# Kernel optimization log

Measured on AMD Instinct MI355X. Metric: run time of the kernel, lower is better.

Reference implementation:

```python
import jax, jax.numpy as jnp
import numpy as np

NUM_EMBEDDINGS = 1024
EMBEDDING_DIM = 256
COMMITMENT_COST = 0.25


def setup_inputs() -> dict:
    key = jax.random.key(0)
    k1, k2 = jax.random.split(key)
    inputs = jax.random.normal(k1, (64, 256, 32, 32), dtype=jnp.float32)
    # nn.Embedding weight init: uniform(-1/K, 1/K)
    embedding = jax.random.uniform(
        k2, (NUM_EMBEDDINGS, EMBEDDING_DIM), dtype=jnp.float32,
        minval=-1.0 / NUM_EMBEDDINGS, maxval=1.0 / NUM_EMBEDDINGS)
    return {"inputs": inputs, "embedding": embedding}


def reference(inputs, embedding):
    # NCHW -> NHWC, flatten to [N, D]
    x = jnp.transpose(inputs, (0, 2, 3, 1))  # [B,H,W,D]
    input_shape = x.shape
    flat = x.reshape(-1, EMBEDDING_DIM)  # [N, D]

    # squared euclidean distances to all codebook entries: [N, K]
    distances = (jnp.sum(flat ** 2, axis=1, keepdims=True)
                 + jnp.sum(embedding ** 2, axis=1)
                 - 2.0 * flat @ embedding.T)
    idx = jnp.argmin(distances, axis=1)  # [N]

    # one-hot encodings (returned output); quantization via gather is
    # mathematically identical to encodings @ embedding
    encodings = jax.nn.one_hot(idx, NUM_EMBEDDINGS, dtype=embedding.dtype)  # [N,K]
    quantized_flat = embedding[idx]  # [N, D]
    quantized = quantized_flat.reshape(input_shape)  # [B,H,W,D]

    e_latent_loss = jnp.mean((jax.lax.stop_gradient(quantized) - x) ** 2)
    q_latent_loss = jnp.mean((quantized - jax.lax.stop_gradient(x)) ** 2)
    loss = q_latent_loss + COMMITMENT_COST * e_latent_loss

    # straight-through estimator
    quantized_st = x + jax.lax.stop_gradient(quantized - x)

    avg_probs = jnp.mean(encodings, axis=0)  # [K]
    perplexity = jnp.exp(-jnp.sum(avg_probs * jnp.log(avg_probs + 1e-10)))

    quantized_out = jnp.transpose(quantized_st, (0, 3, 1, 2))  # NHWC -> NCHW
    return (loss, quantized_out, perplexity, encodings, quantized_flat)
```

## Files before the change

kernel.cpp:

```cpp
#include <hip/hip_runtime.h>
#include <hip/hip_bf16.h>
#include <math.h>

#define NB    64
#define D     256
#define K     1024
#define HW    1024
#define NTOT  65536
#define MARGIN 1e-4f

#define OUT_QOUT   1
#define OUT_PERP   16777217
#define OUT_ENC    16777218
#define OUT_QFLAT  83886082


typedef __attribute__((ext_vector_type(8))) short bf16x8;
typedef __attribute__((ext_vector_type(4))) float f32x4;

__global__ void enorm_kernel(const float* __restrict__ emb, float* __restrict__ enorm) {
    int k = blockIdx.x * 256 + threadIdx.x;
    const float4* row = (const float4*)(emb + (size_t)k * D);
    float s = 0.f;
    #pragma unroll
    for (int q = 0; q < D / 4; q++) {
        float4 v = row[q];
        s += v.x * v.x + v.y * v.y + v.z * v.z + v.w * v.w;
    }
    enorm[k] = s;
}

__global__ void esplit_kernel(const float* __restrict__ emb, ushort* __restrict__ efrag) {
    const int ntg = blockIdx.x;
    const int t = threadIdx.x;
    __shared__ float sEm[16 * 260];

    {
        const int row = t >> 4, seg = t & 15;
        const float4* src = (const float4*)(emb + (size_t)(ntg * 16 + row) * D + seg * 16);
        float4* dst = (float4*)(sEm + row * 260 + seg * 16);
        #pragma unroll
        for (int q = 0; q < 4; q++) dst[q] = src[q];
    }
    __syncthreads();

    const int w = t >> 6, lane = t & 63;
    for (int fb = w; fb < 16; fb += 4) {
        const int h = fb >> 3, dc = fb & 7;
        const float* srcp = sEm + (lane & 15) * 260 + dc * 32 + (lane >> 4) * 8;
        ushort o[8];
        #pragma unroll
        for (int j = 0; j < 8; j++) {
            float x = srcp[j];
            __hip_bfloat16 hb = __float2bfloat16(x);
            if (h == 0) { o[j] = *(ushort*)&hb; }
            else {
                float hf = __bfloat162float(hb);
                __hip_bfloat16 lb = __float2bfloat16(x - hf);
                o[j] = *(ushort*)&lb;
            }
        }
        ushort* dst = efrag + ((size_t)(h * 64 + ntg) * 8 + dc) * 512 + lane * 8;
        *(int4*)dst = *(int4*)o;
    }
}

__global__ __launch_bounds__(256, 2) void score_mfma_kernel(
    const float* __restrict__ in, const ushort* __restrict__ efrag,
    const float* __restrict__ enorm, int* __restrict__ idx,
    int* __restrict__ rcount, int* __restrict__ rlist)
{
    __shared__ ushort sA[32768];

    const int t = threadIdx.x;
    const int n0 = blockIdx.x * 64;
    const int b = n0 >> 10, p0 = n0 & 1023;

    {
        const float* src = in + (size_t)b * (D * HW) + (size_t)t * HW + p0;
        const int quad = (t >> 3) & 3, dc = t >> 5, j = t & 7;
        #pragma unroll
        for (int g = 0; g < 4; g++) {
            float xs[16];
            #pragma unroll
            for (int q = 0; q < 4; q++) {
                float4 v = ((const float4*)src)[g * 4 + q];
                xs[q * 4 + 0] = v.x; xs[q * 4 + 1] = v.y; xs[q * 4 + 2] = v.z; xs[q * 4 + 3] = v.w;
            }
            #pragma unroll
            for (int mm = 0; mm < 16; mm++) {
                float x = xs[mm];
                __hip_bfloat16 hb = __float2bfloat16(x);
                float hf = __bfloat162float(hb);
                __hip_bfloat16 lb = __float2bfloat16(x - hf);
                const int l = mm + 16 * quad;
                sA[((0 * 4 + g) * 8 + dc) * 512 + l * 8 + j] = *(ushort*)&hb;
                sA[((1 * 4 + g) * 8 + dc) * 512 + l * 8 + j] = *(ushort*)&lb;
            }
        }
    }
    __syncthreads();

    const int w = t >> 6, lane = t & 63;

    float rm1 = 3.4e38f, rm2 = 3.4e38f; int ri = 0;

    for (int kp = 0; kp < 4; kp++) {
        float env[4]; int kc[4];
        #pragma unroll
        for (int ntl = 0; ntl < 4; ntl++) {
            kc[ntl] = kp * 256 + (w * 4 + ntl) * 16 + (lane & 15);
            env[ntl] = enorm[kc[ntl]];
        }
        f32x4 acc[4][4];
        #pragma unroll
        for (int mt = 0; mt < 4; mt++)
            #pragma unroll
            for (int ntl = 0; ntl < 4; ntl++) acc[mt][ntl] = (f32x4){0.f, 0.f, 0.f, 0.f};

        bf16x8 bh[4], bl[4], nbh[4], nbl[4];
        {
            #pragma unroll
            for (int ntl = 0; ntl < 4; ntl++) {
                const int ntg = kp * 16 + w * 4 + ntl;
                const size_t off = ((size_t)ntg * 8 + 0) * 512 + lane * 8;
                bh[ntl] = *(const bf16x8*)(efrag + off);
                bl[ntl] = *(const bf16x8*)(efrag + off + 262144);
            }
        }
        for (int dc = 0; dc < 8; dc++) {
            if (dc < 7) {
                #pragma unroll
                for (int ntl = 0; ntl < 4; ntl++) {
                    const int ntg = kp * 16 + w * 4 + ntl;
                    const size_t off = ((size_t)ntg * 8 + dc + 1) * 512 + lane * 8;
                    nbh[ntl] = *(const bf16x8*)(efrag + off);
                    nbl[ntl] = *(const bf16x8*)(efrag + off + 262144);
                }
            }
            #pragma unroll
            for (int mt = 0; mt < 4; mt++) {
                bf16x8 ah = *(const bf16x8*)(sA + ((0 * 4 + mt) * 8 + dc) * 512 + lane * 8);
                bf16x8 al = *(const bf16x8*)(sA + ((1 * 4 + mt) * 8 + dc) * 512 + lane * 8);
                #pragma unroll
                for (int ntl = 0; ntl < 4; ntl++) {
                    acc[mt][ntl] = __builtin_amdgcn_mfma_f32_16x16x32_bf16(al, bh[ntl], acc[mt][ntl], 0, 0, 0);
                    acc[mt][ntl] = __builtin_amdgcn_mfma_f32_16x16x32_bf16(ah, bl[ntl], acc[mt][ntl], 0, 0, 0);
                    acc[mt][ntl] = __builtin_amdgcn_mfma_f32_16x16x32_bf16(ah, bh[ntl], acc[mt][ntl], 0, 0, 0);
                }
            }
            if (dc < 7) {
                #pragma unroll
                for (int ntl = 0; ntl < 4; ntl++) { bh[ntl] = nbh[ntl]; bl[ntl] = nbl[ntl]; }
            }
        }

        #pragma unroll
        for (int mt = 0; mt < 4; mt++)
            #pragma unroll
            for (int r = 0; r < 4; r++) {
                float m1 = 3.4e38f, m2 = 3.4e38f; int i1 = 0;
                #pragma unroll
                for (int ntl = 0; ntl < 4; ntl++) {
                    float s = env[ntl] - 2.0f * acc[mt][ntl][r];
                    if (s < m1) { m2 = m1; m1 = s; i1 = kc[ntl]; }
                    else if (s < m2) m2 = s;
                }
                #pragma unroll
                for (int mask = 1; mask <= 8; mask <<= 1) {
                    float o1 = __shfl_xor(m1, mask, 64);
                    int   oi = __shfl_xor(i1, mask, 64);
                    float o2 = __shfl_xor(m2, mask, 64);
                    float n2 = fminf(fminf(m2, o2), fmaxf(m1, o1));
                    if (o1 < m1 || (o1 == m1 && oi < i1)) { m1 = o1; i1 = oi; }
                    m2 = n2;
                }
                if ((lane & 15) == mt * 4 + r) {
                    float n2 = fminf(fminf(rm2, m2), fmaxf(rm1, m1));
                    if (m1 < rm1 || (m1 == rm1 && i1 < ri)) { rm1 = m1; ri = i1; }
                    rm2 = n2;
                }
            }
    }

    __syncthreads();
    float* sM1 = (float*)sA;
    float* sM2 = sM1 + 256;
    int*   sI  = (int*)(sM2 + 256);
    {
        const int row = ((lane & 15) >> 2) * 16 + (lane >> 4) * 4 + (lane & 3);
        sM1[w * 64 + row] = rm1;
        sM2[w * 64 + row] = rm2;
        sI [w * 64 + row] = ri;
    }
    __syncthreads();
    if (t < 64) {
        float b1 = sM1[t], b2 = sM2[t]; int bi = sI[t];
        #pragma unroll
        for (int ww = 1; ww < 4; ww++) {
            float a1 = sM1[ww * 64 + t], a2 = sM2[ww * 64 + t]; int ai = sI[ww * 64 + t];
            float n2 = fminf(fminf(b2, a2), fmaxf(b1, a1));
            if (a1 < b1 || (a1 == b1 && ai < bi)) { b1 = a1; bi = ai; }
            b2 = n2;
        }
        const int n = n0 + t;
        idx[n] = bi;
        if (b2 - b1 < MARGIN) {
            int pos = atomicAdd(rcount, 1);
            rlist[pos] = n;
        }
    }
}

__global__ void rescue_kernel(const float* __restrict__ in, const float* __restrict__ emb,
                              const int* __restrict__ rcount, const int* __restrict__ rlist,
                              int* __restrict__ idx)
{
    const int wid = blockIdx.x * 4 + (threadIdx.x >> 6);
    const int lane = threadIdx.x & 63;
    const int count = *rcount;
    for (int li = wid; li < count; li += 256 * 4) {
        const int n = rlist[li];
        const int b = n >> 10, p = n & 1023;
        const float* f = in + (size_t)b * (D * HW) + p;
        float fr[4];
        #pragma unroll
        for (int q = 0; q < 4; q++) fr[q] = f[(size_t)(lane + q * 64) * HW];
        double bm = 1e300; int bk = 0;
        for (int kk = 0; kk < 16; kk++) {
            const int k = lane + kk * 64;
            const float* er = emb + (size_t)k * D;
            double s = 0.0;
            #pragma unroll
            for (int q = 0; q < 4; q++) {
                for (int dl = 0; dl < 64; dl++) {
                    double fv = (double)__shfl(fr[q], dl, 64);
                    double ev = (double)er[q * 64 + dl];
                    s += ev * (ev - 2.0 * fv);
                }
            }
            if (s < bm || (s == bm && k < bk)) { bm = s; bk = k; }
        }
        #pragma unroll
        for (int off = 32; off >= 1; off >>= 1) {
            double om = __shfl_xor(bm, off, 64);
            int    ok = __shfl_xor(bk, off, 64);
            if (om < bm || (om == bm && ok < bk)) { bm = om; bk = ok; }
        }
        if (lane == 0) idx[n] = bk;
    }
}

__global__ __launch_bounds__(256) void outputs_kernel(
    const float* __restrict__ in, const float* __restrict__ emb,
    const int* __restrict__ idx, float* __restrict__ out,
    double* __restrict__ lossPartial, int* __restrict__ hist)
{
    __shared__ int skv[32];
    __shared__ float sQ[32 * 260];
    __shared__ double sred[4];

    const int t = threadIdx.x;
    const int n0 = blockIdx.x * 32;
    const int b = n0 >> 10, p0 = n0 & 1023;

    if (t < 32) skv[t] = idx[n0 + t];
    __syncthreads();

    {
        const int r = t >> 3, c0 = (t & 7) * 32;
        const int kv = skv[r];
        const float4* src = (const float4*)(emb + (size_t)kv * D + c0);
        float4* dstL = (float4*)(sQ + r * 260 + c0);
        float4* dstG = (float4*)(out + OUT_QFLAT + (size_t)(n0 + r) * D + c0);
        #pragma unroll
        for (int g = 0; g < 8; g++) {
            float4 v = src[g];
            dstL[g] = v;
            dstG[g] = v;
        }
    }
    if (t < 32) {
        const int kv = skv[t];
        out[OUT_ENC + (size_t)(n0 + t) * K + kv] = 1.0f;
        atomicAdd(&hist[kv], 1);
    }
    __syncthreads();

    const int p = t & 31, dg = t >> 5;
    double acc = 0.0;
    const size_t obase = (size_t)b * (D * HW) + p0 + p;
    #pragma unroll
    for (int dd = 0; dd < 32; dd++) {
        const int d = dg * 32 + dd;
        const float q = sQ[p * 260 + d];
        const float x = in[obase + (size_t)d * HW];
        out[OUT_QOUT + obase + (size_t)d * HW] = q;
        const float df = q - x;
        acc += (double)(df * df);
    }
    #pragma unroll
    for (int off = 32; off >= 1; off >>= 1) acc += __shfl_xor(acc, off, 64);
    if ((t & 63) == 0) sred[t >> 6] = acc;
    __syncthreads();
    if (t == 0) lossPartial[blockIdx.x] = sred[0] + sred[1] + sred[2] + sred[3];
}

__global__ void finalize_kernel(const int* __restrict__ hist, const double* __restrict__ lossPartial,
                                float* __restrict__ out)
{
    const int t = threadIdx.x;
    double s = 0.0;
    #pragma unroll
    for (int q = 0; q < 4; q++) {
        const int c = hist[t + q * 256];
        const double p = (double)c / (double)NTOT;
        s += p * log(p + 1e-10);
    }
    double l = 0.0;
    #pragma unroll
    for (int q = 0; q < 8; q++) l += lossPartial[t + q * 256];
    #pragma unroll
    for (int off = 32; off >= 1; off >>= 1) {
        s += __shfl_xor(s, off, 64);
        l += __shfl_xor(l, off, 64);
    }
    __shared__ double sr[4], lr[4];
    if ((t & 63) == 0) { sr[t >> 6] = s; lr[t >> 6] = l; }
    __syncthreads();
    if (t == 0) {
        out[0] = (float)(1.25 * (lr[0] + lr[1] + lr[2] + lr[3]) / (double)(NTOT * (size_t)D));
        out[OUT_PERP] = (float)exp(-(sr[0] + sr[1] + sr[2] + sr[3]));
    }
}

extern "C" void kernel_launch(void* const* d_in, const int* in_sizes, int n_in,
                              void* d_out, int out_size, void* d_ws, size_t ws_size,
                              hipStream_t stream)
{
    const float* in  = (const float*)d_in[0];
    const float* emb = (const float*)d_in[1];
    float* out = (float*)d_out;
    char* ws = (char*)d_ws;

    int*    rcount      = (int*)(ws + 0);
    int*    hist        = (int*)(ws + 16);
    float*  enorm       = (float*)(ws + 4112);
    int*    idx         = (int*)(ws + 8208);
    int*    rlist       = (int*)(ws + 270352);
    double* lossPartial = (double*)(ws + 532496);
    ushort* efrag       = (ushort*)(ws + 548880);

    hipMemsetAsync(ws, 0, 8208, stream);
    hipMemsetAsync(out + OUT_ENC, 0, (size_t)NTOT * K * sizeof(float), stream);

    enorm_kernel<<<K / 256, 256, 0, stream>>>(emb, enorm);
    esplit_kernel<<<K / 16, 256, 0, stream>>>(emb, efrag);
    score_mfma_kernel<<<NTOT / 64, 256, 0, stream>>>(in, efrag, enorm, idx, rcount, rlist);
    rescue_kernel<<<256, 256, 0, stream>>>(in, emb, rcount, rlist, idx);
    outputs_kernel<<<NTOT / 32, 256, 0, stream>>>(in, emb, idx, out, lossPartial, hist);
    finalize_kernel<<<1, 256, 0, stream>>>(hist, lossPartial, out);
}
```

Measured before the change: 1.010 ms.

## Write one-hot rows densely, shrink score tiles, restructure rescue, tighten margin

Drops the separate full memset of the 256 MB encodings output; the outputs kernel now writes every encoding row itself as dense float4 zeros with the single one set inline, which avoids writing that region twice. The score kernel tiles 32 rows per block instead of 64 with launch bounds raised for 4 blocks per CU, and no longer double-buffers the low-half B fragments, aiming for more occupancy and fewer registers. The rescue kernel accumulates all 16 codebook candidates per lane in one pass over d and uses twice as many blocks. The rescue margin is tightened tenfold, so fewer near-ties get the exact fp64 recheck, which could change argmin results in close cases.

```diff
diff --git a/kernel.cpp b/kernel.cpp
--- a/kernel.cpp
+++ b/kernel.cpp
@@ -7,7 +7,7 @@
 #define K     1024
 #define HW    1024
 #define NTOT  65536
-#define MARGIN 1e-4f
+#define MARGIN 1e-5f
 
 #define OUT_QOUT   1
 #define OUT_PERP   16777217
@@ -65,22 +65,22 @@
     }
 }
 
-__global__ __launch_bounds__(256, 2) void score_mfma_kernel(
+__global__ __launch_bounds__(256, 4) void score_mfma_kernel(
     const float* __restrict__ in, const ushort* __restrict__ efrag,
     const float* __restrict__ enorm, int* __restrict__ idx,
     int* __restrict__ rcount, int* __restrict__ rlist)
 {
-    __shared__ ushort sA[32768];
+    __shared__ ushort sA[16384];
 
     const int t = threadIdx.x;
-    const int n0 = blockIdx.x * 64;
+    const int n0 = blockIdx.x * 32;
     const int b = n0 >> 10, p0 = n0 & 1023;
 
     {
         const float* src = in + (size_t)b * (D * HW) + (size_t)t * HW + p0;
         const int quad = (t >> 3) & 3, dc = t >> 5, j = t & 7;
         #pragma unroll
-        for (int g = 0; g < 4; g++) {
+        for (int g = 0; g < 2; g++) {
             float xs[16];
             #pragma unroll
             for (int q = 0; q < 4; q++) {
@@ -94,8 +94,8 @@
                 float hf = __bfloat162float(hb);
                 __hip_bfloat16 lb = __float2bfloat16(x - hf);
                 const int l = mm + 16 * quad;
-                sA[((0 * 4 + g) * 8 + dc) * 512 + l * 8 + j] = *(ushort*)&hb;
-                sA[((1 * 4 + g) * 8 + dc) * 512 + l * 8 + j] = *(ushort*)&lb;
+                sA[((0 * 2 + g) * 8 + dc) * 512 + l * 8 + j] = *(ushort*)&hb;
+                sA[((1 * 2 + g) * 8 + dc) * 512 + l * 8 + j] = *(ushort*)&lb;
             }
         }
     }
@@ -106,57 +106,52 @@
     float rm1 = 3.4e38f, rm2 = 3.4e38f; int ri = 0;
 
     for (int kp = 0; kp < 4; kp++) {
+        f32x4 acc[2][4];
+        #pragma unroll
+        for (int mt = 0; mt < 2; mt++)
+            #pragma unroll
+            for (int ntl = 0; ntl < 4; ntl++) acc[mt][ntl] = (f32x4){0.f, 0.f, 0.f, 0.f};
+
+        bf16x8 bh[4], nbh[4];
+        #pragma unroll
+        for (int ntl = 0; ntl < 4; ntl++) {
+            const int ntg = kp * 16 + w * 4 + ntl;
+            bh[ntl] = *(const bf16x8*)(efrag + ((size_t)ntg * 8 + 0) * 512 + lane * 8);
+        }
+        for (int dc = 0; dc < 8; dc++) {
+            bf16x8 bl[4];
+            #pragma unroll
+            for (int ntl = 0; ntl < 4; ntl++) {
+                const int ntg = kp * 16 + w * 4 + ntl;
+                const size_t off = ((size_t)ntg * 8 + dc) * 512 + lane * 8;
+                bl[ntl] = *(const bf16x8*)(efrag + off + 262144);
+                if (dc < 7) nbh[ntl] = *(const bf16x8*)(efrag + off + 512);
+            }
+            #pragma unroll
+            for (int mt = 0; mt < 2; mt++) {
+                bf16x8 ah = *(const bf16x8*)(sA + ((0 * 2 + mt) * 8 + dc) * 512 + lane * 8);
+                bf16x8 al = *(const bf16x8*)(sA + ((1 * 2 + mt) * 8 + dc) * 512 + lane * 8);
+                #pragma unroll
+                for (int ntl = 0; ntl < 4; ntl++) {
+                    acc[mt][ntl] = __builtin_amdgcn_mfma_f32_16x16x32_bf16(al, bh[ntl], acc[mt][ntl], 0, 0, 0);
+                    acc[mt][ntl] = __builtin_amdgcn_mfma_f32_16x16x32_bf16(ah, bh[ntl], acc[mt][ntl], 0, 0, 0);
+                    acc[mt][ntl] = __builtin_amdgcn_mfma_f32_16x16x32_bf16(ah, bl[ntl], acc[mt][ntl], 0, 0, 0);
+                }
+            }
+            if (dc < 7) {
+                #pragma unroll
+                for (int ntl = 0; ntl < 4; ntl++) bh[ntl] = nbh[ntl];
+            }
+        }
+
         float env[4]; int kc[4];
         #pragma unroll
         for (int ntl = 0; ntl < 4; ntl++) {
             kc[ntl] = kp * 256 + (w * 4 + ntl) * 16 + (lane & 15);
             env[ntl] = enorm[kc[ntl]];
         }
-        f32x4 acc[4][4];
-        #pragma unroll
-        for (int mt = 0; mt < 4; mt++)
-            #pragma unroll
-            for (int ntl = 0; ntl < 4; ntl++) acc[mt][ntl] = (f32x4){0.f, 0.f, 0.f, 0.f};
-
-        bf16x8 bh[4], bl[4], nbh[4], nbl[4];
-        {
-            #pragma unroll
-            for (int ntl = 0; ntl < 4; ntl++) {
-                const int ntg = kp * 16 + w * 4 + ntl;
-                const size_t off = ((size_t)ntg * 8 + 0) * 512 + lane * 8;
-                bh[ntl] = *(const bf16x8*)(efrag + off);
-                bl[ntl] = *(const bf16x8*)(efrag + off + 262144);
-            }
-        }
-        for (int dc = 0; dc < 8; dc++) {
-            if (dc < 7) {
-                #pragma unroll
-                for (int ntl = 0; ntl < 4; ntl++) {
-                    const int ntg = kp * 16 + w * 4 + ntl;
-                    const size_t off = ((size_t)ntg * 8 + dc + 1) * 512 + lane * 8;
-                    nbh[ntl] = *(const bf16x8*)(efrag + off);
-                    nbl[ntl] = *(const bf16x8*)(efrag + off + 262144);
-                }
-            }
-            #pragma unroll
-            for (int mt = 0; mt < 4; mt++) {
-                bf16x8 ah = *(const bf16x8*)(sA + ((0 * 4 + mt) * 8 + dc) * 512 + lane * 8);
-                bf16x8 al = *(const bf16x8*)(sA + ((1 * 4 + mt) * 8 + dc) * 512 + lane * 8);
-                #pragma unroll
-                for (int ntl = 0; ntl < 4; ntl++) {
-                    acc[mt][ntl] = __builtin_amdgcn_mfma_f32_16x16x32_bf16(al, bh[ntl], acc[mt][ntl], 0, 0, 0);
-                    acc[mt][ntl] = __builtin_amdgcn_mfma_f32_16x16x32_bf16(ah, bl[ntl], acc[mt][ntl], 0, 0, 0);
-                    acc[mt][ntl] = __builtin_amdgcn_mfma_f32_16x16x32_bf16(ah, bh[ntl], acc[mt][ntl], 0, 0, 0);
-                }
-            }
-            if (dc < 7) {
-                #pragma unroll
-                for (int ntl = 0; ntl < 4; ntl++) { bh[ntl] = nbh[ntl]; bl[ntl] = nbl[ntl]; }
-            }
-        }
-
-        #pragma unroll
-        for (int mt = 0; mt < 4; mt++)
+        #pragma unroll
+        for (int mt = 0; mt < 2; mt++)
             #pragma unroll
             for (int r = 0; r < 4; r++) {
                 float m1 = 3.4e38f, m2 = 3.4e38f; int i1 = 0;
@@ -185,20 +180,20 @@
 
     __syncthreads();
     float* sM1 = (float*)sA;
-    float* sM2 = sM1 + 256;
-    int*   sI  = (int*)(sM2 + 256);
-    {
+    float* sM2 = sM1 + 128;
+    int*   sI  = (int*)(sM2 + 128);
+    if ((lane & 15) < 8) {
         const int row = ((lane & 15) >> 2) * 16 + (lane >> 4) * 4 + (lane & 3);
-        sM1[w * 64 + row] = rm1;
-        sM2[w * 64 + row] = rm2;
-        sI [w * 64 + row] = ri;
-    }
-    __syncthreads();
-    if (t < 64) {
+        sM1[w * 32 + row] = rm1;
+        sM2[w * 32 + row] = rm2;
+        sI [w * 32 + row] = ri;
+    }
+    __syncthreads();
+    if (t < 32) {
         float b1 = sM1[t], b2 = sM2[t]; int bi = sI[t];
         #pragma unroll
         for (int ww = 1; ww < 4; ww++) {
-            float a1 = sM1[ww * 64 + t], a2 = sM2[ww * 64 + t]; int ai = sI[ww * 64 + t];
+            float a1 = sM1[ww * 32 + t], a2 = sM2[ww * 32 + t]; int ai = sI[ww * 32 + t];
             float n2 = fminf(fminf(b2, a2), fmaxf(b1, a1));
             if (a1 < b1 || (a1 == b1 && ai < bi)) { b1 = a1; bi = ai; }
             b2 = n2;
@@ -219,27 +214,32 @@
     const int wid = blockIdx.x * 4 + (threadIdx.x >> 6);
     const int lane = threadIdx.x & 63;
     const int count = *rcount;
-    for (int li = wid; li < count; li += 256 * 4) {
+    for (int li = wid; li < count; li += 512 * 4) {
         const int n = rlist[li];
         const int b = n >> 10, p = n & 1023;
         const float* f = in + (size_t)b * (D * HW) + p;
         float fr[4];
         #pragma unroll
         for (int q = 0; q < 4; q++) fr[q] = f[(size_t)(lane + q * 64) * HW];
+        double s[16];
+        #pragma unroll
+        for (int kk = 0; kk < 16; kk++) s[kk] = 0.0;
+        for (int q = 0; q < 4; q++) {
+            for (int dl = 0; dl < 64; dl++) {
+                const double fv = (double)__shfl(fr[q], dl, 64);
+                const int d = q * 64 + dl;
+                #pragma unroll
+                for (int kk = 0; kk < 16; kk++) {
+                    const double ev = (double)emb[(size_t)(lane + kk * 64) * D + d];
+                    s[kk] += ev * (ev - 2.0 * fv);
+                }
+            }
+        }
         double bm = 1e300; int bk = 0;
+        #pragma unroll
         for (int kk = 0; kk < 16; kk++) {
             const int k = lane + kk * 64;
-            const float* er = emb + (size_t)k * D;
-            double s = 0.0;
-            #pragma unroll
-            for (int q = 0; q < 4; q++) {
-                for (int dl = 0; dl < 64; dl++) {
-                    double fv = (double)__shfl(fr[q], dl, 64);
-                    double ev = (double)er[q * 64 + dl];
-                    s += ev * (ev - 2.0 * fv);
-                }
-            }
-            if (s < bm || (s == bm && k < bk)) { bm = s; bk = k; }
+            if (s[kk] < bm) { bm = s[kk]; bk = k; }
         }
         #pragma unroll
         for (int off = 32; off >= 1; off >>= 1) {
@@ -280,11 +280,18 @@
             dstG[g] = v;
         }
     }
-    if (t < 32) {
-        const int kv = skv[t];
-        out[OUT_ENC + (size_t)(n0 + t) * K + kv] = 1.0f;
-        atomicAdd(&hist[kv], 1);
-    }
+    {
+        float* encBase = out + OUT_ENC + (size_t)n0 * K;
+        const int c0 = t * 4;
+        #pragma unroll 4
+        for (int r = 0; r < 32; r++) {
+            const int kv = skv[r];
+            float4 v = make_float4(0.f, 0.f, 0.f, 0.f);
+            if (kv >= c0 && kv < c0 + 4) ((float*)&v)[kv - c0] = 1.0f;
+            *(float4*)(encBase + (size_t)r * K + c0) = v;
+        }
+    }
+    if (t < 32) atomicAdd(&hist[skv[t]], 1);
     __syncthreads();
 
     const int p = t & 31, dg = t >> 5;
@@ -352,12 +359,11 @@
     ushort* efrag       = (ushort*)(ws + 548880);
 
     hipMemsetAsync(ws, 0, 8208, stream);
-    hipMemsetAsync(out + OUT_ENC, 0, (size_t)NTOT * K * sizeof(float), stream);
 
     enorm_kernel<<<K / 256, 256, 0, stream>>>(emb, enorm);
     esplit_kernel<<<K / 16, 256, 0, stream>>>(emb, efrag);
-    score_mfma_kernel<<<NTOT / 64, 256, 0, stream>>>(in, efrag, enorm, idx, rcount, rlist);
-    rescue_kernel<<<256, 256, 0, stream>>>(in, emb, rcount, rlist, idx);
+    score_mfma_kernel<<<NTOT / 32, 256, 0, stream>>>(in, efrag, enorm, idx, rcount, rlist);
+    rescue_kernel<<<512, 256, 0, stream>>>(in, emb, rcount, rlist, idx);
     outputs_kernel<<<NTOT / 32, 256, 0, stream>>>(in, emb, idx, out, lossPartial, hist);
     finalize_kernel<<<1, 256, 0, stream>>>(hist, lossPartial, out);
 }
```

Result: slower. 1.240 ms (+22.8%).
